# Kernel tuning notes

Measured on AMD Instinct MI355X. Metric: run time of the kernel, lower is better.

## Reference

```python
import jax, jax.numpy as jnp
import numpy as np

VOCAB, EMBED, HID = 50257, 512, 512
B, SRC = 128, 128


def setup_inputs() -> dict:
    key = jax.random.key(0)
    ks = jax.random.split(key, 16)
    s = 0.02
    emb_tab = jax.random.normal(ks[0], (VOCAB, EMBED), jnp.float32) * s
    emb_tab = emb_tab.at[0].set(0.0)  # padding_idx=0
    return {
        "x": jax.random.randint(ks[1], (B,), 0, VOCAB),
        "decoder_hidden": jax.random.normal(ks[2], (1, B, HID), jnp.float32),
        "source_lens": jax.random.randint(ks[3], (B,), 1, SRC + 1),
        "encoder_outputs": jax.random.normal(ks[4], (B, SRC, HID), jnp.float32),
        "context_vec": jax.random.normal(ks[5], (B, HID), jnp.float32),
        "embedding": emb_tab,
        "w_ih": jax.random.normal(ks[6], (3 * HID, HID + EMBED), jnp.float32) * s,
        "w_hh": jax.random.normal(ks[7], (3 * HID, HID), jnp.float32) * s,
        "b_ih": jax.random.normal(ks[8], (3 * HID,), jnp.float32) * s,
        "b_hh": jax.random.normal(ks[9], (3 * HID,), jnp.float32) * s,
        "Wa": jax.random.normal(ks[10], (HID, HID), jnp.float32) * s,
        "Wc": jax.random.normal(ks[11], (HID, 2 * HID), jnp.float32) * s,
        "fc1_w": jax.random.normal(ks[12], (VOCAB, HID), jnp.float32) * s,
        "fc1_b": jax.random.normal(ks[13], (VOCAB,), jnp.float32) * s,
    }


def _gru_step(inp, h, w_ih, w_hh, b_ih, b_hh):
    # inp: [B, I], h: [B, H] -> h': [B, H]  (PyTorch GRU gate order: r, z, n)
    gi = inp @ w_ih.T + b_ih
    gh = h @ w_hh.T + b_hh
    i_r, i_z, i_n = jnp.split(gi, 3, axis=1)
    h_r, h_z, h_n = jnp.split(gh, 3, axis=1)
    r = jax.nn.sigmoid(i_r + h_r)
    z = jax.nn.sigmoid(i_z + h_z)
    n = jnp.tanh(i_n + r * h_n)
    return (1.0 - z) * n + z * h


def reference(x, decoder_hidden, source_lens, encoder_outputs, context_vec,
              embedding, w_ih, w_hh, b_ih, b_hh, Wa, Wc, fc1_w, fc1_b):
    # embedding lookup (dropout is identity in eval mode)
    emb = embedding[x]                                    # [B, E]
    rnn_in = jnp.concatenate([emb, context_vec], axis=1)  # [B, E+H]
    h = _gru_step(rnn_in, decoder_hidden[0], w_ih, w_hh, b_ih, b_hh)  # [B, H]
    hidden = h[None]                                      # [1, B, H]

    # Luong-style attention (scores laid out [src_len, B] as in original)
    q = h @ Wa.T                                          # [B, H]
    attn_scores = jnp.einsum('bsh,bh->sb', encoder_outputs, q)  # [S, B]
    seq_range = jnp.arange(encoder_outputs.shape[1])      # [S]
    enc_mask = (seq_range[None, :] < source_lens[:, None]).T    # [S, B]
    masked = enc_mask.astype(attn_scores.dtype) * attn_scores
    masked = jnp.where(masked == 0, jnp.asarray(-1e10, masked.dtype), masked)
    a = jax.nn.softmax(masked, axis=0)                    # [S, B]
    ctx = jnp.einsum('sb,bsh->bh', a, encoder_outputs)    # [B, H]
    ctx = jnp.tanh(jnp.concatenate([ctx, h], axis=1) @ Wc.T)    # [B, H]

    logits = ctx @ fc1_w.T + fc1_b                        # [B, V]
    log_probs = jax.nn.log_softmax(logits, axis=1)
    return log_probs, hidden, a, ctx
```

## Files before the change

kernel.cpp:

```cpp
#include <hip/hip_runtime.h>

#define VOCAB 50257
#define EMBED 512
#define HID   512
#define B     128
#define SRC   128
#define NT393 393

typedef __attribute__((ext_vector_type(8))) short short8;
typedef __attribute__((ext_vector_type(4))) float f32x4;

__device__ __forceinline__ unsigned f2bf(float x) {
    unsigned u = __builtin_bit_cast(unsigned, x);
    return (u + 0x7fffu + ((u >> 16) & 1u)) >> 16;
}
__device__ __forceinline__ unsigned pk2(float lo, float hi) {
    return f2bf(lo) | (f2bf(hi) << 16);
}
__device__ __forceinline__ uint4 pk8(const float* p) {
    uint4 r;
    r.x = pk2(p[0], p[1]); r.y = pk2(p[2], p[3]);
    r.z = pk2(p[4], p[5]); r.w = pk2(p[6], p[7]);
    return r;
}
__device__ __forceinline__ uint4 pk8v(float4 a, float4 b) {
    uint4 r;
    r.x = pk2(a.x, a.y); r.y = pk2(a.z, a.w);
    r.z = pk2(b.x, b.y); r.w = pk2(b.z, b.w);
    return r;
}
__device__ __forceinline__ void gll16(const void* g, void* l) {
    __builtin_amdgcn_global_load_lds(
        (const __attribute__((address_space(1))) void*)g,
        (__attribute__((address_space(3))) void*)l, 16, 0, 0);
}


__global__ void k_embed_pack(const int* __restrict__ x, const float* __restrict__ ctxv,
                             const float* __restrict__ emb, const float* __restrict__ h0,
                             uint4* __restrict__ apk_rnn, uint4* __restrict__ apk_h0) {
    __shared__ float buf[1024];
    __shared__ float hbuf[512];
    const int b = blockIdx.x, t = threadIdx.x;
    const int row = x[b];
    if (t < 128) {
        ((float4*)buf)[t]  = ((const float4*)(emb + (size_t)row * EMBED))[t];
        ((float4*)hbuf)[t] = ((const float4*)(h0 + (size_t)b * HID))[t];
    } else {
        ((float4*)buf)[t] = ((const float4*)(ctxv + (size_t)b * HID))[t - 128];
    }
    __syncthreads();
    const int mt = b >> 4, lb = b & 15;
    if (t < 128) {
        int kc = t >> 4, ksl = (t >> 2) & 3, kg = t & 3;
        apk_rnn[((kc * 8 + mt) * 4 + ksl) * 64 + kg * 16 + lb] = pk8(&buf[t * 8]);
    } else if (t < 192) {
        int i = t - 128;
        int kc = i >> 4, ksl = (i >> 2) & 3, kg = i & 3;
        apk_h0[((kc * 8 + mt) * 4 + ksl) * 64 + kg * 16 + lb] = pk8(&hbuf[i * 8]);
    }
}

template <int N, int K, int ACT, int HASB, int PACK>
__global__ __launch_bounds__(256, 2) void k_gemm_ks(
        const uint4* __restrict__ apk, const float* __restrict__ W,
        const float* __restrict__ bias, float* __restrict__ C,
        uint4* __restrict__ apk_out) {
    __shared__ float red[4][128][16];
    const int tid = threadIdx.x, lane = tid & 63, wv = tid >> 6;
    const int n0 = blockIdx.x * 16;
    const int ncol = n0 + (lane & 15);
    const int nc = ncol < N ? ncol : N - 1;
    const int kg = lane >> 4;
    constexpr int SPW = K / 128;
    f32x4 acc[8];
#pragma unroll
    for (int mt = 0; mt < 8; ++mt) acc[mt] = (f32x4)0.f;
    const float4* W4 = (const float4*)W;
    const size_t wb = (size_t)nc * (K / 4) + kg * 2;
#pragma unroll
    for (int s = 0; s < SPW; ++s) {
        const int ks = wv * SPW + s;
        float4 w0 = W4[wb + ks * 8];
        float4 w1 = W4[wb + ks * 8 + 1];
        short8 bf = __builtin_bit_cast(short8, pk8v(w0, w1));
        const uint4* ap = apk + (((ks >> 2) * 8) * 4 + (ks & 3)) * 64 + lane;
#pragma unroll
        for (int mt = 0; mt < 8; ++mt) {
            short8 af = __builtin_bit_cast(short8, ap[mt * 256]);
            acc[mt] = __builtin_amdgcn_mfma_f32_16x16x32_bf16(af, bf, acc[mt], 0, 0, 0);
        }
    }
#pragma unroll
    for (int mt = 0; mt < 8; ++mt)
#pragma unroll
        for (int j = 0; j < 4; ++j)
            red[wv][mt * 16 + kg * 4 + j][lane & 15] = acc[mt][j];
    __syncthreads();
#pragma unroll
    for (int i = 0; i < 8; ++i) {
        int o = tid + i * 256;
        int r = o >> 4, c = o & 15;
        float v = red[0][r][c] + red[1][r][c] + red[2][r][c] + red[3][r][c];
        if (HASB) v += bias[n0 + c];
        if (ACT) v = tanhf(v);
        C[(size_t)r * N + n0 + c] = v;
        if (PACK) red[0][r][c] = v;
    }
    if constexpr (PACK) {
        __syncthreads();
        int r = tid >> 1, hf = tid & 1;
        float tmp[8];
#pragma unroll
        for (int z = 0; z < 8; ++z) tmp[z] = red[0][r][hf * 8 + z];
        int k0 = n0 + hf * 8;
        int kc = k0 >> 7, ksl = (k0 >> 5) & 3, kg2 = (k0 >> 3) & 3;
        apk_out[((kc * 8 + (r >> 4)) * 4 + ksl) * 64 + kg2 * 16 + (r & 15)] = pk8(tmp);
    }
}

__global__ void k_gru(const float* __restrict__ gi, const float* __restrict__ gh,
                      const float* __restrict__ h0, float* __restrict__ h,
                      uint4* __restrict__ apk_h) {
    __shared__ float hsh[256];
    const int t = threadIdx.x;
    const int idx = blockIdx.x * 256 + t;
    const int b = blockIdx.x >> 1, half = blockIdx.x & 1;
    const int j = half * 256 + t;
    const float* gib = gi + (size_t)b * 1536;
    const float* ghb = gh + (size_t)b * 1536;
    float ir = gib[j], iz = gib[512 + j], inn = gib[1024 + j];
    float hr = ghb[j], hz = ghb[512 + j], hn = ghb[1024 + j];
    float r = 1.f / (1.f + expf(-(ir + hr)));
    float z = 1.f / (1.f + expf(-(iz + hz)));
    float nn = tanhf(inn + r * hn);
    float hv = (1.f - z) * nn + z * h0[idx];
    h[idx] = hv;
    hsh[t] = hv;
    __syncthreads();
    if (t < 32) {
        int k0 = half * 256 + t * 8;
        int kc = k0 >> 7, ksl = (k0 >> 5) & 3, kg = (k0 >> 3) & 3;
        apk_h[((kc * 8 + (b >> 4)) * 4 + ksl) * 64 + kg * 16 + (b & 15)] = pk8(&hsh[t * 8]);
    }
}

__global__ __launch_bounds__(512) void k_attn(const float* __restrict__ enc,
        const float* __restrict__ q, const int* __restrict__ lens,
        const float* __restrict__ h, float* __restrict__ a_out,
        uint4* __restrict__ apk_cat) {
    __shared__ float qs[512];
    __shared__ float red[128];
    __shared__ float aw[128];
    __shared__ float catsh[1024];
    const int b = blockIdx.x, t = threadIdx.x;
    qs[t] = q[(size_t)b * 512 + t];
    __syncthreads();
    const int srow = t >> 2, part = t & 3;
    const float* ep = enc + ((size_t)b * SRC + srow) * 512 + part * 128;
    float s = 0.f;
#pragma unroll
    for (int k4 = 0; k4 < 32; ++k4) {
        float4 e = ((const float4*)ep)[k4];
        float4 qq = *(const float4*)&qs[part * 128 + k4 * 4];
        s = fmaf(e.x, qq.x, fmaf(e.y, qq.y, fmaf(e.z, qq.z, fmaf(e.w, qq.w, s))));
    }
    s += __shfl_xor(s, 1);
    s += __shfl_xor(s, 2);
    if (part == 0) {
        int len = lens[b];
        float val = (srow < len) ? s : 0.f;
        if (val == 0.f) val = -1e10f;
        red[srow] = val;
        aw[srow] = val;
    }
    __syncthreads();
    for (int off = 64; off > 0; off >>= 1) {
        if (t < off) red[t] = fmaxf(red[t], red[t + off]);
        __syncthreads();
    }
    float mx = red[0];
    __syncthreads();
    if (t < 128) { float e = expf(aw[t] - mx); aw[t] = e; red[t] = e; }
    __syncthreads();
    for (int off = 64; off > 0; off >>= 1) {
        if (t < off) red[t] += red[t + off];
        __syncthreads();
    }
    float denom = red[0];
    if (t < 128) {
        float av = aw[t] / denom;
        aw[t] = av;
        a_out[(size_t)t * B + b] = av;
    }
    __syncthreads();
    float a0 = 0.f;
    const float* e2 = enc + (size_t)b * (SRC * 512) + t;
#pragma unroll 4
    for (int s2 = 0; s2 < SRC; ++s2) a0 = fmaf(aw[s2], e2[(size_t)s2 * 512], a0);
    catsh[t] = a0;
    catsh[512 + t] = h[(size_t)b * 512 + t];
    __syncthreads();
    if (t < 128) {
        int kc = t >> 4, ksl = (t >> 2) & 3, kg = t & 3;
        apk_cat[((kc * 8 + (b >> 4)) * 4 + ksl) * 64 + kg * 16 + (b & 15)] =
            pk8(&catsh[t * 8]);
    }
}

#define FC1_LOADC(dst, wbase, c)                                        \
    _Pragma("unroll")                                                   \
    for (int q = 0; q < 4; ++q) {                                       \
        dst[2 * q]     = W4[(wbase) + (size_t)((4 * (c) + q) * 8)];     \
        dst[2 * q + 1] = W4[(wbase) + (size_t)((4 * (c) + q) * 8 + 1)]; \
    }
#define FC1_CONS(src, c)                                                \
    _Pragma("unroll")                                                   \
    for (int q = 0; q < 4; ++q) {                                       \
        short8 bf = __builtin_bit_cast(short8, pk8v(src[2 * q], src[2 * q + 1])); \
        const int base = ((c) * 32 + q) * 64 + lane;                    \
        _Pragma("unroll")                                               \
        for (int mt = 0; mt < 8; ++mt) {                                \
            short8 af = __builtin_bit_cast(short8, As[base + mt * 256]);\
            acc[mt] = __builtin_amdgcn_mfma_f32_16x16x32_bf16(af, bf, acc[mt], 0, 0, 0); \
        }                                                               \
    }

__global__ __launch_bounds__(512, 2) void k_fc1p(
        const uint4* __restrict__ apk, const float* __restrict__ W,
        const float* __restrict__ bias, float* __restrict__ C,
        float2* __restrict__ pout) {
    __shared__ uint4 As[8192];
    __shared__ float2 pms[2][8][128];
    const int tid = threadIdx.x, lane = tid & 63, wv = tid >> 6;
    const int kg = lane >> 4;
#pragma unroll
    for (int it = 0; it < 16; ++it)
        gll16(apk + it * 512 + tid, As + it * 512 + tid);
    __syncthreads();
    const float4* W4 = (const float4*)W;

    float4 Ab[8], Bb[8];
    int nt0 = blockIdx.x;
    {
        int ncol0 = nt0 * 128 + wv * 16 + (lane & 15);
        size_t wb0 = (size_t)(ncol0 < VOCAB ? ncol0 : VOCAB - 1) * 128 + kg * 2;
        FC1_LOADC(Ab, wb0, 0);
    }
    int pb = 0;
    size_t wb;
    {
        int ncol0 = nt0 * 128 + wv * 16 + (lane & 15);
        wb = (size_t)(ncol0 < VOCAB ? ncol0 : VOCAB - 1) * 128 + kg * 2;
    }
    for (int nt = nt0; nt < NT393; nt += 256) {
        const int ncol = nt * 128 + wv * 16 + (lane & 15);
        const bool valid = ncol < VOCAB;
        const int nc = valid ? ncol : VOCAB - 1;
        const int ntn = (nt + 256 < NT393) ? nt + 256 : NT393 - 1;
        const int ncoln = ntn * 128 + wv * 16 + (lane & 15);
        const size_t wbn = (size_t)(ncoln < VOCAB ? ncoln : VOCAB - 1) * 128 + kg * 2;
        f32x4 acc[8];
#pragma unroll
        for (int mt = 0; mt < 8; ++mt) acc[mt] = (f32x4)0.f;
        FC1_LOADC(Bb, wb, 1);
        FC1_CONS(Ab, 0);
        FC1_LOADC(Ab, wb, 2);
        FC1_CONS(Bb, 1);
        FC1_LOADC(Bb, wb, 3);
        FC1_CONS(Ab, 2);
        FC1_LOADC(Ab, wbn, 0);
        FC1_CONS(Bb, 3);

        float bb = bias[nc];
#pragma unroll
        for (int mt = 0; mt < 8; ++mt) {
#pragma unroll
            for (int j = 0; j < 4; ++j) {
                float v = acc[mt][j] + bb;
                int row = mt * 16 + kg * 4 + j;
                if (valid) C[(size_t)row * VOCAB + ncol] = v;
                if (pout) {
                    float val = valid ? v : -1e30f;
                    float m16 = val;
                    m16 = fmaxf(m16, __shfl_xor(m16, 1));
                    m16 = fmaxf(m16, __shfl_xor(m16, 2));
                    m16 = fmaxf(m16, __shfl_xor(m16, 4));
                    m16 = fmaxf(m16, __shfl_xor(m16, 8));
                    float e = valid ? __expf(val - m16) : 0.f;
                    e += __shfl_xor(e, 1);
                    e += __shfl_xor(e, 2);
                    e += __shfl_xor(e, 4);
                    e += __shfl_xor(e, 8);
                    if ((lane & 15) == 0) pms[pb][wv][row] = make_float2(m16, e);
                }
            }
        }
        if (pout) {
            __syncthreads();
            if (tid < 128) {
                float2 p = pms[pb][0][tid];
                float m = p.x, s = p.y;
#pragma unroll
                for (int w = 1; w < 8; ++w) {
                    float2 p2 = pms[pb][w][tid];
                    float mm = fmaxf(m, p2.x);
                    s = s * __expf(m - mm) + p2.y * __expf(p2.x - mm);
                    m = mm;
                }
                pout[(size_t)tid * NT393 + nt] = make_float2(m, s);
            }
            pb ^= 1;
        }
        wb = wbn;
    }
}

__global__ __launch_bounds__(256) void k_lse_final(const float2* __restrict__ pout,
                                                   float* __restrict__ L, int nblk) {
    const int row = blockIdx.x, t = threadIdx.x;
    float m = -1e30f, s = 0.f;
    for (int i = t; i < nblk; i += 256) {
        float2 p = pout[(size_t)row * nblk + i];
        float mm = fmaxf(m, p.x);
        s = s * __expf(m - mm) + p.y * __expf(p.x - mm);
        m = mm;
    }
    __shared__ float sm[256], ss[256];
    sm[t] = m; ss[t] = s; __syncthreads();
    for (int off = 128; off > 0; off >>= 1) {
        if (t < off) {
            float m2 = sm[t + off], s2 = ss[t + off];
            float mm = fmaxf(sm[t], m2);
            ss[t] = ss[t] * __expf(sm[t] - mm) + s2 * __expf(m2 - mm);
            sm[t] = mm;
        }
        __syncthreads();
    }
    if (t == 0) L[row] = sm[0] + logf(ss[0]);
}

__global__ __launch_bounds__(512) void k_lsub(float* __restrict__ logits,
                                              const float* __restrict__ L) {
    const int b = blockIdx.y;
    const float l = L[b];
    float* row = logits + (size_t)b * VOCAB;
    int c0 = (blockIdx.x * 512 + threadIdx.x) * 4;
    if (c0 + 4 <= VOCAB) {
        float4 x = *(float4*)(row + c0);
        x.x -= l; x.y -= l; x.z -= l; x.w -= l;
        *(float4*)(row + c0) = x;
    } else {
        for (int c = c0; c < VOCAB; ++c) row[c] -= l;
    }
}

__global__ __launch_bounds__(1024) void k_lse_sub(float* __restrict__ logits) {
    const int b = blockIdx.x, t = threadIdx.x;
    float* row = logits + (size_t)b * VOCAB;
    const int N4 = VOCAB >> 2;
    float m = -1e30f, s = 0.f;
    for (int i = t; i < N4; i += 1024) {
        float4 x = ((const float4*)row)[i];
        float xs[4] = {x.x, x.y, x.z, x.w};
#pragma unroll
        for (int j = 0; j < 4; ++j) {
            float v = xs[j];
            if (v > m) { s = s * __expf(m - v) + 1.f; m = v; }
            else        s += __expf(v - m);
        }
    }
    if (t == 0) {
        float v = row[VOCAB - 1];
        if (v > m) { s = s * __expf(m - v) + 1.f; m = v; }
        else        s += __expf(v - m);
    }
    __shared__ float sm[1024], ss[1024];
    sm[t] = m; ss[t] = s;
    __syncthreads();
    for (int off = 512; off > 0; off >>= 1) {
        if (t < off) {
            float m2 = sm[t + off], s2 = ss[t + off];
            float mm = fmaxf(sm[t], m2);
            ss[t] = ss[t] * __expf(sm[t] - mm) + s2 * __expf(m2 - mm);
            sm[t] = mm;
        }
        __syncthreads();
    }
    __shared__ float Lsh;
    if (t == 0) Lsh = sm[0] + logf(ss[0]);
    __syncthreads();
    float L = Lsh;
    for (int i = t; i < N4; i += 1024) {
        float4 x = ((const float4*)row)[i];
        x.x -= L; x.y -= L; x.z -= L; x.w -= L;
        ((float4*)row)[i] = x;
    }
    if (t == 0) row[VOCAB - 1] -= L;
}

extern "C" void kernel_launch(void* const* d_in, const int* in_sizes, int n_in,
                              void* d_out, int out_size, void* d_ws, size_t ws_size,
                              hipStream_t stream) {
    const int*   x    = (const int*)d_in[0];
    const float* h0   = (const float*)d_in[1];
    const int*   lens = (const int*)d_in[2];
    const float* enc  = (const float*)d_in[3];
    const float* ctxv = (const float*)d_in[4];
    const float* emb  = (const float*)d_in[5];
    const float* wih  = (const float*)d_in[6];
    const float* whh  = (const float*)d_in[7];
    const float* bih  = (const float*)d_in[8];
    const float* bhh  = (const float*)d_in[9];
    const float* Wa   = (const float*)d_in[10];
    const float* Wc   = (const float*)d_in[11];
    const float* fc1w = (const float*)d_in[12];
    const float* fc1b = (const float*)d_in[13];

    float* out     = (float*)d_out;
    float* outLogp = out;
    float* outHid  = out + (size_t)B * VOCAB;
    float* outA    = outHid + (size_t)B * HID;
    float* outCtx  = outA + (size_t)SRC * B;

    float* gi = outLogp;
    float* gh = gi + B * 1536;
    float* q  = gh + B * 1536;
    uint4* apk_rnn = (uint4*)(q + B * HID);
    uint4* apk_h0  = apk_rnn + 16384;
    uint4* apk_h   = apk_h0 + 8192;
    uint4* apk_cat = apk_h + 8192;

    uint4*  apk_ctx = (uint4*)d_ws;
    size_t  off_pout = 131072;
    size_t  off_L    = off_pout + (size_t)B * NT393 * sizeof(float2);
    bool bigws = ws_size >= off_L + 512;
    float2* pout = bigws ? (float2*)((char*)d_ws + off_pout) : nullptr;
    float*  Lb   = bigws ? (float*)((char*)d_ws + off_L) : nullptr;

    k_embed_pack<<<dim3(B), dim3(256), 0, stream>>>(x, ctxv, emb, h0, apk_rnn, apk_h0);
    k_gemm_ks<1536, 1024, 0, 1, 0><<<dim3(96), dim3(256), 0, stream>>>(
        apk_rnn, wih, bih, gi, nullptr);
    k_gemm_ks<1536, 512, 0, 1, 0><<<dim3(96), dim3(256), 0, stream>>>(
        apk_h0, whh, bhh, gh, nullptr);
    k_gru<<<dim3(256), dim3(256), 0, stream>>>(gi, gh, h0, outHid, apk_h);
    k_gemm_ks<512, 512, 0, 0, 0><<<dim3(32), dim3(256), 0, stream>>>(
        apk_h, Wa, nullptr, q, nullptr);
    k_attn<<<dim3(B), dim3(512), 0, stream>>>(enc, q, lens, outHid, outA, apk_cat);
    k_gemm_ks<512, 1024, 1, 0, 1><<<dim3(32), dim3(256), 0, stream>>>(
        apk_cat, Wc, nullptr, outCtx, apk_ctx);
    if (bigws) {
        k_fc1p<<<dim3(256), dim3(512), 0, stream>>>(apk_ctx, fc1w, fc1b, outLogp, pout);
        k_lse_final<<<dim3(B), dim3(256), 0, stream>>>(pout, Lb, NT393);
        k_lsub<<<dim3(25, B), dim3(512), 0, stream>>>(outLogp, Lb);
    } else {
        k_fc1p<<<dim3(256), dim3(512), 0, stream>>>(apk_ctx, fc1w, fc1b, outLogp, nullptr);
        k_lse_sub<<<dim3(B), dim3(1024), 0, stream>>>(outLogp);
    }
}
```

Before: 123.8 us.

## Pre-convert fc1 weights to packed bf16 in idle blocks of earlier kernels

Adds extra blocks to the small GRU, attention and Wc kernels that convert fc1_w (float32) into an MFMA-ready packed bf16 layout in workspace. The conversion overlaps with the underutilised earlier stages. A new fc1 kernel then reads the pre-packed weights directly, halving its weight traffic and dropping conversion work from the critical path. It adds roughly 100 MB of extra memory traffic (fp32 read plus bf16 write), spread across earlier launches, and needs a large workspace; otherwise it falls back to the old path.

```diff
diff --git a/kernel.cpp b/kernel.cpp
--- a/kernel.cpp
+++ b/kernel.cpp
@@ -6,6 +6,7 @@
 #define B     128
 #define SRC   128
 #define NT393 393
+#define WPKG  3144
 
 typedef __attribute__((ext_vector_type(8))) short short8;
 typedef __attribute__((ext_vector_type(4))) float f32x4;
@@ -35,6 +36,16 @@
         (__attribute__((address_space(3))) void*)l, 16, 0, 0);
 }
 
+
+
+__device__ __forceinline__ void wconv_wave(const float* __restrict__ fw,
+        uint4* __restrict__ wpk, int r0, int r1, int gw, int gstride, int lane) {
+    for (int n = r0 + gw; n < r1; n += gstride) {
+        const float4* src = (const float4*)(fw + (size_t)n * 512);
+        uint4 f = pk8v(src[2 * lane], src[2 * lane + 1]);
+        wpk[(size_t)(n >> 4) * 1024 + (lane >> 2) * 64 + (lane & 3) * 16 + (n & 15)] = f;
+    }
+}
 
 __global__ void k_embed_pack(const int* __restrict__ x, const float* __restrict__ ctxv,
                              const float* __restrict__ emb, const float* __restrict__ h0,
@@ -65,9 +76,17 @@
 __global__ __launch_bounds__(256, 2) void k_gemm_ks(
         const uint4* __restrict__ apk, const float* __restrict__ W,
         const float* __restrict__ bias, float* __restrict__ C,
-        uint4* __restrict__ apk_out) {
+        uint4* __restrict__ apk_out,
+        const float* __restrict__ fw, uint4* __restrict__ wpk,
+        int wr0, int wr1, int nown) {
+    const int tid = threadIdx.x, lane = tid & 63, wv = tid >> 6;
+    if ((int)blockIdx.x >= nown) {
+        if (wpk) wconv_wave(fw, wpk, wr0, wr1,
+                            ((int)blockIdx.x - nown) * 4 + wv,
+                            ((int)gridDim.x - nown) * 4, lane);
+        return;
+    }
     __shared__ float red[4][128][16];
-    const int tid = threadIdx.x, lane = tid & 63, wv = tid >> 6;
     const int n0 = blockIdx.x * 16;
     const int ncol = n0 + (lane & 15);
     const int nc = ncol < N ? ncol : N - 1;
@@ -148,12 +167,21 @@
 __global__ __launch_bounds__(512) void k_attn(const float* __restrict__ enc,
         const float* __restrict__ q, const int* __restrict__ lens,
         const float* __restrict__ h, float* __restrict__ a_out,
-        uint4* __restrict__ apk_cat) {
+        uint4* __restrict__ apk_cat,
+        const float* __restrict__ fw, uint4* __restrict__ wpk,
+        int wr0, int wr1, int nown) {
+    const int t = threadIdx.x;
+    if ((int)blockIdx.x >= nown) {
+        if (wpk) wconv_wave(fw, wpk, wr0, wr1,
+                            ((int)blockIdx.x - nown) * 8 + (t >> 6),
+                            ((int)gridDim.x - nown) * 8, t & 63);
+        return;
+    }
     __shared__ float qs[512];
     __shared__ float red[128];
     __shared__ float aw[128];
     __shared__ float catsh[1024];
-    const int b = blockIdx.x, t = threadIdx.x;
+    const int b = blockIdx.x;
     qs[t] = q[(size_t)b * 512 + t];
     __syncthreads();
     const int srow = t >> 2, part = t & 3;
@@ -205,6 +233,79 @@
         int kc = t >> 4, ksl = (t >> 2) & 3, kg = t & 3;
         apk_cat[((kc * 8 + (b >> 4)) * 4 + ksl) * 64 + kg * 16 + (b & 15)] =
             pk8(&catsh[t * 8]);
+    }
+}
+
+__global__ __launch_bounds__(512, 1) void k_fc1w(
+        const uint4* __restrict__ apk, const uint4* __restrict__ wpk,
+        const float* __restrict__ bias, float* __restrict__ C,
+        float2* __restrict__ pout) {
+    __shared__ uint4 As[8192];
+    __shared__ float2 pms[2][8][128];
+    const int tid = threadIdx.x, lane = tid & 63, wv = tid >> 6;
+    const int kg = lane >> 4;
+#pragma unroll
+    for (int it = 0; it < 16; ++it)
+        gll16(apk + it * 512 + tid, As + it * 512 + tid);
+    __syncthreads();
+    int pb = 0;
+    for (int nt = blockIdx.x; nt < NT393; nt += 256) {
+        const int cb = nt * 8 + wv;
+        const int ncol = cb * 16 + (lane & 15);
+        const bool valid = ncol < VOCAB;
+        const uint4* wp = wpk + (size_t)cb * 1024 + lane;
+        uint4 wf[16];
+#pragma unroll
+        for (int ks = 0; ks < 16; ++ks) wf[ks] = wp[ks * 64];
+        f32x4 acc[8];
+#pragma unroll
+        for (int mt = 0; mt < 8; ++mt) acc[mt] = (f32x4)0.f;
+#pragma unroll
+        for (int ks = 0; ks < 16; ++ks) {
+            short8 bf = __builtin_bit_cast(short8, wf[ks]);
+            const int base = ((ks >> 2) * 32 + (ks & 3)) * 64 + lane;
+#pragma unroll
+            for (int mt = 0; mt < 8; ++mt) {
+                short8 af = __builtin_bit_cast(short8, As[base + mt * 256]);
+                acc[mt] = __builtin_amdgcn_mfma_f32_16x16x32_bf16(af, bf, acc[mt], 0, 0, 0);
+            }
+        }
+        float bb = bias[valid ? ncol : VOCAB - 1];
+#pragma unroll
+        for (int mt = 0; mt < 8; ++mt) {
+#pragma unroll
+            for (int j = 0; j < 4; ++j) {
+                float v = acc[mt][j] + bb;
+                int row = mt * 16 + kg * 4 + j;
+                if (valid) C[(size_t)row * VOCAB + ncol] = v;
+                float val = valid ? v : -1e30f;
+                float m16 = val;
+                m16 = fmaxf(m16, __shfl_xor(m16, 1));
+                m16 = fmaxf(m16, __shfl_xor(m16, 2));
+                m16 = fmaxf(m16, __shfl_xor(m16, 4));
+                m16 = fmaxf(m16, __shfl_xor(m16, 8));
+                float e = valid ? __expf(val - m16) : 0.f;
+                e += __shfl_xor(e, 1);
+                e += __shfl_xor(e, 2);
+                e += __shfl_xor(e, 4);
+                e += __shfl_xor(e, 8);
+                if ((lane & 15) == 0) pms[pb][wv][row] = make_float2(m16, e);
+            }
+        }
+        __syncthreads();
+        if (tid < 128) {
+            float2 p = pms[pb][0][tid];
+            float m = p.x, s = p.y;
+#pragma unroll
+            for (int w = 1; w < 8; ++w) {
+                float2 p2 = pms[pb][w][tid];
+                float mm = fmaxf(m, p2.x);
+                s = s * __expf(m - mm) + p2.y * __expf(p2.x - mm);
+                m = mm;
+            }
+            pout[(size_t)tid * NT393 + nt] = make_float2(m, s);
+        }
+        pb ^= 1;
     }
 }
 
@@ -239,20 +340,15 @@
         gll16(apk + it * 512 + tid, As + it * 512 + tid);
     __syncthreads();
     const float4* W4 = (const float4*)W;
-
     float4 Ab[8], Bb[8];
     int nt0 = blockIdx.x;
-    {
-        int ncol0 = nt0 * 128 + wv * 16 + (lane & 15);
-        size_t wb0 = (size_t)(ncol0 < VOCAB ? ncol0 : VOCAB - 1) * 128 + kg * 2;
-        FC1_LOADC(Ab, wb0, 0);
-    }
-    int pb = 0;
     size_t wb;
     {
         int ncol0 = nt0 * 128 + wv * 16 + (lane & 15);
         wb = (size_t)(ncol0 < VOCAB ? ncol0 : VOCAB - 1) * 128 + kg * 2;
-    }
+        FC1_LOADC(Ab, wb, 0);
+    }
+    int pb = 0;
     for (int nt = nt0; nt < NT393; nt += 256) {
         const int ncol = nt * 128 + wv * 16 + (lane & 15);
         const bool valid = ncol < VOCAB;
@@ -271,7 +367,6 @@
         FC1_CONS(Ab, 2);
         FC1_LOADC(Ab, wbn, 0);
         FC1_CONS(Bb, 3);
-
         float bb = bias[nc];
 #pragma unroll
         for (int mt = 0; mt < 8; ++mt) {
@@ -434,22 +529,31 @@
     uint4*  apk_ctx = (uint4*)d_ws;
     size_t  off_pout = 131072;
     size_t  off_L    = off_pout + (size_t)B * NT393 * sizeof(float2);
-    bool bigws = ws_size >= off_L + 512;
+    size_t  off_wpk  = 534016;
+    size_t  wpk_bytes = (size_t)WPKG * 1024 * 16;
+    bool bigws  = ws_size >= off_L + 512;
+    bool bigws2 = ws_size >= off_wpk + wpk_bytes;
     float2* pout = bigws ? (float2*)((char*)d_ws + off_pout) : nullptr;
     float*  Lb   = bigws ? (float*)((char*)d_ws + off_L) : nullptr;
+    uint4*  wpk  = bigws2 ? (uint4*)((char*)d_ws + off_wpk) : nullptr;
 
     k_embed_pack<<<dim3(B), dim3(256), 0, stream>>>(x, ctxv, emb, h0, apk_rnn, apk_h0);
-    k_gemm_ks<1536, 1024, 0, 1, 0><<<dim3(96), dim3(256), 0, stream>>>(
-        apk_rnn, wih, bih, gi, nullptr);
-    k_gemm_ks<1536, 512, 0, 1, 0><<<dim3(96), dim3(256), 0, stream>>>(
-        apk_h0, whh, bhh, gh, nullptr);
+    k_gemm_ks<1536, 1024, 0, 1, 0><<<dim3(wpk ? 800 : 96), dim3(256), 0, stream>>>(
+        apk_rnn, wih, bih, gi, nullptr, fc1w, wpk, 0, 14000, 96);
+    k_gemm_ks<1536, 512, 0, 1, 0><<<dim3(wpk ? 800 : 96), dim3(256), 0, stream>>>(
+        apk_h0, whh, bhh, gh, nullptr, fc1w, wpk, 14000, 28000, 96);
     k_gru<<<dim3(256), dim3(256), 0, stream>>>(gi, gh, h0, outHid, apk_h);
     k_gemm_ks<512, 512, 0, 0, 0><<<dim3(32), dim3(256), 0, stream>>>(
-        apk_h, Wa, nullptr, q, nullptr);
-    k_attn<<<dim3(B), dim3(512), 0, stream>>>(enc, q, lens, outHid, outA, apk_cat);
-    k_gemm_ks<512, 1024, 1, 0, 1><<<dim3(32), dim3(256), 0, stream>>>(
-        apk_cat, Wc, nullptr, outCtx, apk_ctx);
-    if (bigws) {
+        apk_h, Wa, nullptr, q, nullptr, nullptr, nullptr, 0, 0, 32);
+    k_attn<<<dim3(wpk ? 768 : B), dim3(512), 0, stream>>>(
+        enc, q, lens, outHid, outA, apk_cat, fc1w, wpk, 28000, 39000, B);
+    k_gemm_ks<512, 1024, 1, 0, 1><<<dim3(wpk ? 768 : 32), dim3(256), 0, stream>>>(
+        apk_cat, Wc, nullptr, outCtx, apk_ctx, fc1w, wpk, 39000, VOCAB, 32);
+    if (bigws2) {
+        k_fc1w<<<dim3(256), dim3(512), 0, stream>>>(apk_ctx, wpk, fc1b, outLogp, pout);
+        k_lse_final<<<dim3(B), dim3(256), 0, stream>>>(pout, Lb, NT393);
+        k_lsub<<<dim3(25, B), dim3(512), 0, stream>>>(outLogp, Lb);
+    } else if (bigws) {
         k_fc1p<<<dim3(256), dim3(512), 0, stream>>>(apk_ctx, fc1w, fc1b, outLogp, pout);
         k_lse_final<<<dim3(B), dim3(256), 0, stream>>>(pout, Lb, NT393);
         k_lsub<<<dim3(25, B), dim3(512), 0, stream>>>(outLogp, Lb);
```

Measured after the change: 136.2 us. +10.0%, slower.
